# Kernel tuning notes

Measured on AMD Instinct MI355X. Metric: run time of the kernel, lower is better.

## Reference

```python
import jax, jax.numpy as jnp
import numpy as np

BATCH = 32768
DIM = 256
NUM_LATENTS = 4096
ENTROPY_WEIGHT = 0.1
VQ_BETA = 0.25
EPS = 1e-9


def _l2_normalize(v, axis=-1, eps=1e-12):
    # matches torch F.normalize(dim=-1)
    n = jnp.linalg.norm(v, axis=axis, keepdims=True)
    return v / jnp.maximum(n, eps)


def setup_inputs() -> dict:
    key = jax.random.key(0)
    kx, kc = jax.random.split(key)
    x = jax.random.normal(kx, (BATCH, DIM), dtype=jnp.float32)
    # codebook initialized uniform(-bound, bound) then row-normalized, as in __init__
    bound = (3.0 / DIM) ** 0.5
    cb = jax.random.uniform(kc, (NUM_LATENTS, DIM), dtype=jnp.float32,
                            minval=-bound, maxval=bound)
    codebook = _l2_normalize(cb)
    return {"x": x, "codebook": codebook}


def reference(x, codebook):
    # cosine-distance nearest-code lookup
    x_norm = _l2_normalize(x)                       # [B, D]
    cb_norm = _l2_normalize(codebook)               # [K, D]
    distance = -jnp.einsum('bd,kd->bk', x_norm, cb_norm)  # [B, K]
    # dropout p=0.0 -> identity
    indices = jnp.argmin(distance, axis=-1)         # [B] int
    z = codebook[indices]                           # [B, D] gather

    # straight-through estimator
    z_q = x + jax.lax.stop_gradient(z - x)

    commit_loss = jnp.mean((x - jax.lax.stop_gradient(z)) ** 2)
    q_loss = jnp.mean((z - jax.lax.stop_gradient(x)) ** 2)

    # entropy of codebook usage
    counts = jnp.bincount(indices, length=NUM_LATENTS).astype(jnp.float32)
    probs = counts / counts.sum()
    entropy = -jnp.sum(probs * jnp.log(jnp.clip(probs, EPS)))
    entropy_loss = -entropy

    vq_loss = q_loss + VQ_BETA * commit_loss + ENTROPY_WEIGHT * entropy_loss
    return (z_q, vq_loss, q_loss, commit_loss, entropy_loss, entropy, indices)
```

## Files before the change

kernel.cpp:

```cpp
#include <hip/hip_runtime.h>
#include <math.h>

#define BATCH 32768
#define DIM   256
#define NLAT  4096

typedef _Float16 f16x8 __attribute__((ext_vector_type(8)));
typedef float    f32x16 __attribute__((ext_vector_type(16)));

#define WS_CBH    0u
#define WS_CBINV  2097152u
#define WS_KEYS   2113536u
#define WS_HIST   4210688u

__device__ inline float kdec(uint key) {
  return __uint_as_float(key & 0xFFFFF000u);
}

__device__ inline void gload_lds16(const void* g, void* l) {
  __builtin_amdgcn_global_load_lds(
      (const __attribute__((address_space(1))) void*)g,
      (__attribute__((address_space(3))) void*)l, 16, 0, 0);
}

__global__ __launch_bounds__(256) void prep1_kernel(
    const float* __restrict__ cb, float* __restrict__ cbinv,
    int* __restrict__ hist) {
  int bid = blockIdx.x;
  if (bid < 1024) {
    int w = threadIdx.x >> 6, l = threadIdx.x & 63;
    int row = bid * 4 + w;
    const float4* cr = (const float4*)(cb + (size_t)row * DIM);
    float4 v = cr[l];
    float s = v.x * v.x + v.y * v.y + v.z * v.z + v.w * v.w;
    #pragma unroll
    for (int m = 32; m; m >>= 1) s += __shfl_xor(s, m, 64);
    if (l == 0) cbinv[row] = 1.0f / fmaxf(sqrtf(s), 1e-12f);
  } else {
    for (int k = threadIdx.x; k < NLAT; k += 256) hist[k] = 0;
  }
}

__global__ __launch_bounds__(256) void prep2_kernel(
    const float* __restrict__ x, const float* __restrict__ cb,
    const float* __restrict__ cbinv, uint4* __restrict__ cbhf4,
    uint4* __restrict__ xhf4) {
  int bid = blockIdx.x, tid = threadIdx.x;
  if (bid < 512) {
    int gid = bid * 256 + tid;
    int frag = gid >> 6, lane = gid & 63;
    int rf = frag & 1, ts = frag >> 1, sl = ts & 15, t = ts >> 4;
    int row = t * 64 + rf * 32 + (lane & 31);
    int e4 = sl * 4 + (lane >> 5) * 2;
    const float4* cr = (const float4*)(cb + (size_t)row * DIM);
    float inv = cbinv[row];
    float4 a = cr[e4], b = cr[e4 + 1];
    union { _Float16 h[8]; uint4 u; } pk;
    pk.h[0] = (_Float16)(a.x * inv); pk.h[1] = (_Float16)(a.y * inv);
    pk.h[2] = (_Float16)(a.z * inv); pk.h[3] = (_Float16)(a.w * inv);
    pk.h[4] = (_Float16)(b.x * inv); pk.h[5] = (_Float16)(b.y * inv);
    pk.h[6] = (_Float16)(b.z * inv); pk.h[7] = (_Float16)(b.w * inv);
    cbhf4[gid] = pk.u;
  } else {
    int o = (bid - 512) * 256 + tid;
    int rowgrp = o >> 10, rem = o & 1023;
    int sl = rem >> 6, rem2 = rem & 63;
    int lhh = rem2 >> 5, l31r = rem2 & 31;
    int row = rowgrp * 32 + l31r;
    int c = sl * 2 + lhh;
    const float4* xs = (const float4*)x;
    float4 a = xs[(size_t)row * 64 + c * 2];
    float4 b = xs[(size_t)row * 64 + c * 2 + 1];
    union { _Float16 h[8]; uint4 u; } pk;
    pk.h[0] = (_Float16)a.x; pk.h[1] = (_Float16)a.y;
    pk.h[2] = (_Float16)a.z; pk.h[3] = (_Float16)a.w;
    pk.h[4] = (_Float16)b.x; pk.h[5] = (_Float16)b.y;
    pk.h[6] = (_Float16)b.z; pk.h[7] = (_Float16)b.w;
    xhf4[o] = pk.u;
  }
}

__global__ __launch_bounds__(256, 2) void vq_gemm_kernel(
    const char* __restrict__ xhf, const char* __restrict__ cbhf,
    uint* __restrict__ keys) {
  __shared__ __align__(16) char smem[65536];

  const int tid = threadIdx.x;
  const int w = tid >> 6, l = tid & 63;
  const int l31 = l & 31, lh = l >> 5;
  const int bb = blockIdx.x >> 2, q = blockIdx.x & 3;
  const int wrow0 = bb * 256 + w * 64;
  const int cbase = q * 1024;
  const uint lh4u = (uint)(lh << 2);

  f16x8 xf[16][2];
  #pragma unroll
  for (int fc = 0; fc < 2; ++fc) {
    const char* xb = xhf + (size_t)(bb * 8 + w * 2 + fc) * 16384
                   + (size_t)l * 16;
    #pragma unroll
    for (int s2 = 0; s2 < 16; ++s2)
      xf[s2][fc] = *(const f16x8*)(xb + s2 * 1024);
  }

  const char* qbase = cbhf + (size_t)q * 524288;
  auto STAGE = [&](int bufoff, int t) {
    const char* src = qbase + t * 32768 + (size_t)tid * 16;
    char* dst = smem + bufoff + w * 1024;
    #pragma unroll
    for (int s = 0; s < 8; ++s)
      gload_lds16(src + s * 4096, dst + s * 4096);
  };

  STAGE(0, 0);
  asm volatile("s_waitcnt vmcnt(0)" ::: "memory");
  __syncthreads();

  uint k1[2] = {0, 0}, k2[2] = {0, 0}, k3[2] = {0, 0};
  int curoff = 0;

  #pragma unroll 1
  for (int t = 0; t < 16; ++t) {
    if (t < 15) STAGE(curoff ^ 32768, t + 1);

    f32x16 acc[2][2];
    #pragma unroll
    for (int rf = 0; rf < 2; ++rf)
      #pragma unroll
      for (int fc = 0; fc < 2; ++fc)
        #pragma unroll
        for (int r = 0; r < 16; ++r) acc[rf][fc][r] = 32.0f;

    const char* bp = smem + curoff + (size_t)l * 16;
    #pragma unroll
    for (int sl = 0; sl < 16; ++sl) {
      f16x8 a0 = *(const f16x8*)(bp + (sl * 2) * 1024);
      f16x8 a1 = *(const f16x8*)(bp + (sl * 2 + 1) * 1024);
      #pragma unroll
      for (int fc = 0; fc < 2; ++fc) {
        acc[0][fc] = __builtin_amdgcn_mfma_f32_32x32x16_f16(
            a0, xf[sl][fc], acc[0][fc], 0, 0, 0);
        acc[1][fc] = __builtin_amdgcn_mfma_f32_32x32x16_f16(
            a1, xf[sl][fc], acc[1][fc], 0, 0, 0);
      }
    }

    const uint scode = (uint)(cbase + t * 64);
    #pragma unroll
    for (int fc = 0; fc < 2; ++fc) {
      #pragma unroll
      for (int rf = 0; rf < 2; ++rf) {
        #pragma unroll
        for (int r = 0; r < 16; ++r) {
          const uint cr = (uint)(rf * 32 + (r & 3) + 8 * (r >> 2));
          uint key = (__float_as_uint(acc[rf][fc][r]) & 0xFFFFF000u)
                   | scode | cr | lh4u;
          uint m1 = max(k1[fc], key), n1 = min(k1[fc], key); k1[fc] = m1;
          uint m2 = max(k2[fc], n1),  n2 = min(k2[fc], n1);  k2[fc] = m2;
          k3[fc] = max(k3[fc], n2);
        }
      }
    }

    asm volatile("s_waitcnt vmcnt(0)" ::: "memory");
    __syncthreads();
    curoff ^= 32768;
  }

  #pragma unroll
  for (int fc = 0; fc < 2; ++fc) {
    uint a1 = k1[fc], a2 = k2[fc], a3 = k3[fc];
    uint o1 = __shfl_xor(a1, 32, 64);
    uint o2 = __shfl_xor(a2, 32, 64);
    uint o3 = __shfl_xor(a3, 32, 64);
    uint a4 = 0;
    #pragma unroll
    for (int e = 0; e < 3; ++e) {
      uint o = (e == 0) ? o1 : (e == 1) ? o2 : o3;
      uint m = max(a1, o), n = min(a1, o); a1 = m;
      m = max(a2, n); n = min(a2, n); a2 = m;
      m = max(a3, n); n = min(a3, n); a3 = m;
      a4 = max(a4, n);
    }
    if (lh == 0) {
      uint4 kv; kv.x = a1; kv.y = a2; kv.z = a3; kv.w = a4;
      *(uint4*)(keys + (size_t)(wrow0 + fc * 32 + l31) * 16 + q * 4) = kv;
    }
  }
}

__global__ __launch_bounds__(256) void rescore_kernel(
    const float* __restrict__ x, const float* __restrict__ cb,
    const float* __restrict__ cbinv, const uint* __restrict__ keys,
    float* __restrict__ zq, float* __restrict__ out_idx,
    int* __restrict__ hist, double* __restrict__ psse) {
  __shared__ float part[4];
  int tid = threadIdx.x, w = tid >> 6, l = tid & 63;
  int row = blockIdx.x * 4 + w;
  const float4* xr = (const float4*)(x + (size_t)row * DIM);
  float4 xv = xr[l];
  float s0 = xv.x * xv.x + xv.y * xv.y + xv.z * xv.z + xv.w * xv.w;
  #pragma unroll
  for (int m = 32; m; m >>= 1) s0 += __shfl_xor(s0, m, 64);
  float xnorm = sqrtf(s0);
  float xinv = 1.0f / fmaxf(xnorm, 1e-12f);

  uint key = keys[row * 16 + (l & 15)];
  uint kmax = key;
  #pragma unroll
  for (int m = 1; m < 16; m <<= 1) {
    uint o = __shfl_xor(kmax, m, 64);
    kmax = (o > kmax) ? o : kmax;
  }
  float dmax = kdec(kmax);
  float thr = dmax - 2.0f * (3e-3f * xnorm);
  bool inwin = (kdec(key) >= thr) && (l < 16);
  unsigned long long mask = __ballot(inwin);
  int besti;
  if (__popcll(mask) == 1) {
    besti = (int)(kmax & 0xFFFu);
  } else {
    float bestv = -3e38f; besti = 0x7fffffff;
    unsigned long long mm = mask;
    while (mm) {
      int b = __ffsll(mm) - 1; mm &= mm - 1;
      int ci = (int)(__shfl(key, b, 64) & 0xFFFu);
      float cbi = cbinv[ci];
      const float4* cr = (const float4*)(cb + (size_t)ci * DIM);
      float4 cv = cr[l];
      float d = (xv.x * xinv) * (cv.x * cbi) + (xv.y * xinv) * (cv.y * cbi)
              + (xv.z * xinv) * (cv.z * cbi) + (xv.w * xinv) * (cv.w * cbi);
      #pragma unroll
      for (int m = 32; m; m >>= 1) d += __shfl_xor(d, m, 64);
      bool better = (d > bestv) || (d == bestv && ci < besti);
      bestv = better ? d : bestv;
      besti = better ? ci : besti;
    }
  }

  float4 zv = ((const float4*)(cb + (size_t)besti * DIM))[l];
  float4 o;
  o.x = xv.x + (zv.x - xv.x); o.y = xv.y + (zv.y - xv.y);
  o.z = xv.z + (zv.z - xv.z); o.w = xv.w + (zv.w - xv.w);
  ((float4*)(zq + (size_t)row * DIM))[l] = o;
  float dx = xv.x - zv.x, dy = xv.y - zv.y, dz = xv.z - zv.z, dw = xv.w - zv.w;
  float s = dx * dx + dy * dy + dz * dz + dw * dw;
  #pragma unroll
  for (int m = 32; m; m >>= 1) s += __shfl_xor(s, m, 64);
  if (l == 0) part[w] = s;
  __syncthreads();
  if (tid == 0)
    psse[blockIdx.x] = (double)((part[0] + part[1]) + (part[2] + part[3]));
  if (l == 0) {
    atomicAdd(&hist[besti], 1);
    out_idx[row] = (float)besti;
  }
}

__global__ __launch_bounds__(256) void finalize_kernel(
    const int* __restrict__ hist, const double* __restrict__ psse,
    float* __restrict__ outs) {
  int tid = threadIdx.x;
  double e = 0.0, s = 0.0;
  for (int k = tid; k < NLAT; k += 256) {
    int c = hist[k];
    if (c > 0) {
      float p = (float)c * (1.0f / 32768.0f);
      e += (double)(p * logf(p));
    }
  }
  for (int k = tid; k < BATCH / 4; k += 256) s += psse[k];
  #pragma unroll
  for (int off = 32; off; off >>= 1) {
    e += __shfl_xor(e, off, 64);
    s += __shfl_xor(s, off, 64);
  }
  __shared__ double pe[4], ps[4];
  int w = tid >> 6, l = tid & 63;
  if (l == 0) { pe[w] = e; ps[w] = s; }
  __syncthreads();
  if (tid == 0) {
    double H = -((pe[0] + pe[1]) + (pe[2] + pe[3]));
    double sse = (ps[0] + ps[1]) + (ps[2] + ps[3]);
    double qv = sse * (1.0 / ((double)BATCH * (double)DIM));
    float qf = (float)qv;
    float Hf = (float)H;
    float ent_loss = -Hf;
    float vq = qf + 0.25f * qf + 0.1f * ent_loss;
    outs[0] = vq;
    outs[1] = qf;
    outs[2] = qf;
    outs[3] = ent_loss;
    outs[4] = Hf;
  }
}

extern "C" void kernel_launch(void* const* d_in, const int* in_sizes, int n_in,
                              void* d_out, int out_size, void* d_ws, size_t ws_size,
                              hipStream_t stream) {
  const float* x  = (const float*)d_in[0];
  const float* cb = (const float*)d_in[1];

  float* out     = (float*)d_out;
  float* zq      = out;
  float* scalars = out + (size_t)BATCH * DIM;
  float* oidx    = scalars + 5;

  char* wsb = (char*)d_ws;
  ushort* cbhf  = (ushort*)(wsb + WS_CBH);
  float*  cbinv = (float*)(wsb + WS_CBINV);
  uint*   keys  = (uint*)(wsb + WS_KEYS);
  int*    hist  = (int*)(wsb + WS_HIST);
  double* psse  = (double*)(wsb + WS_CBH);

  ushort* xhf = (ushort*)d_out;

  prep1_kernel<<<1025, 256, 0, stream>>>(cb, cbinv, hist);
  prep2_kernel<<<4608, 256, 0, stream>>>(x, cb, cbinv,
                                         (uint4*)cbhf, (uint4*)xhf);
  vq_gemm_kernel<<<512, 256, 0, stream>>>((const char*)xhf,
                                          (const char*)cbhf, keys);
  rescore_kernel<<<BATCH / 4, 256, 0, stream>>>(x, cb, cbinv, keys,
                                                zq, oidx, hist, psse);
  finalize_kernel<<<1, 256, 0, stream>>>(hist, psse, scalars);
}
```

Baseline: 200.8 us.

## Deepen GEMM codebook pipeline to four half-tile buffers and coalesce x conversion

The GEMM kernel now stages the codebook in 16KB half-tiles across a four-slot LDS ring with three stages in flight, using partial vmcnt waits instead of full drains. MFMA sections run at raised wave priority. The x fp16 conversion now reads rows contiguously and transposes the fragment layout through LDS, using fewer blocks, so global reads are coalesced. This adds more barriers per tile and relies on the vmcnt counting being correct for the ring.

```diff
diff --git a/kernel.cpp b/kernel.cpp
--- a/kernel.cpp
+++ b/kernel.cpp
@@ -46,8 +46,29 @@
     const float* __restrict__ cbinv, uint4* __restrict__ cbhf4,
     uint4* __restrict__ xhf4) {
   int bid = blockIdx.x, tid = threadIdx.x;
-  if (bid < 512) {
-    int gid = bid * 256 + tid;
+  if (bid < 1024) {
+    __shared__ __align__(16) uint4 lds[1024];
+    const float4* xs = (const float4*)x + (size_t)bid * 2048;
+    #pragma unroll
+    for (int k = 0; k < 4; ++k) {
+      int g = tid * 4 + k;
+      float4 a = xs[g * 2];
+      float4 b = xs[g * 2 + 1];
+      union { _Float16 h[8]; uint4 u; } pk;
+      pk.h[0] = (_Float16)a.x; pk.h[1] = (_Float16)a.y;
+      pk.h[2] = (_Float16)a.z; pk.h[3] = (_Float16)a.w;
+      pk.h[4] = (_Float16)b.x; pk.h[5] = (_Float16)b.y;
+      pk.h[6] = (_Float16)b.z; pk.h[7] = (_Float16)b.w;
+      int row31 = g >> 5, c = g & 31;
+      lds[(c >> 1) * 64 + (c & 1) * 32 + row31] = pk.u;
+    }
+    __syncthreads();
+    uint4* outp = xhf4 + (size_t)bid * 1024;
+    #pragma unroll
+    for (int k = 0; k < 4; ++k)
+      outp[tid * 4 + k] = lds[tid * 4 + k];
+  } else {
+    int gid = (bid - 1024) * 256 + tid;
     int frag = gid >> 6, lane = gid & 63;
     int rf = frag & 1, ts = frag >> 1, sl = ts & 15, t = ts >> 4;
     int row = t * 64 + rf * 32 + (lane & 31);
@@ -61,22 +82,6 @@
     pk.h[4] = (_Float16)(b.x * inv); pk.h[5] = (_Float16)(b.y * inv);
     pk.h[6] = (_Float16)(b.z * inv); pk.h[7] = (_Float16)(b.w * inv);
     cbhf4[gid] = pk.u;
-  } else {
-    int o = (bid - 512) * 256 + tid;
-    int rowgrp = o >> 10, rem = o & 1023;
-    int sl = rem >> 6, rem2 = rem & 63;
-    int lhh = rem2 >> 5, l31r = rem2 & 31;
-    int row = rowgrp * 32 + l31r;
-    int c = sl * 2 + lhh;
-    const float4* xs = (const float4*)x;
-    float4 a = xs[(size_t)row * 64 + c * 2];
-    float4 b = xs[(size_t)row * 64 + c * 2 + 1];
-    union { _Float16 h[8]; uint4 u; } pk;
-    pk.h[0] = (_Float16)a.x; pk.h[1] = (_Float16)a.y;
-    pk.h[2] = (_Float16)a.z; pk.h[3] = (_Float16)a.w;
-    pk.h[4] = (_Float16)b.x; pk.h[5] = (_Float16)b.y;
-    pk.h[6] = (_Float16)b.z; pk.h[7] = (_Float16)b.w;
-    xhf4[o] = pk.u;
   }
 }
 
@@ -104,45 +109,70 @@
   }
 
   const char* qbase = cbhf + (size_t)q * 524288;
-  auto STAGE = [&](int bufoff, int t) {
-    const char* src = qbase + t * 32768 + (size_t)tid * 16;
-    char* dst = smem + bufoff + w * 1024;
-    #pragma unroll
-    for (int s = 0; s < 8; ++s)
+  auto STAGE = [&](int h) {
+    const char* src = qbase + h * 16384 + (size_t)tid * 16;
+    char* dst = smem + (h & 3) * 16384 + w * 1024;
+    #pragma unroll
+    for (int s = 0; s < 4; ++s)
       gload_lds16(src + s * 4096, dst + s * 4096);
   };
 
-  STAGE(0, 0);
   asm volatile("s_waitcnt vmcnt(0)" ::: "memory");
-  __syncthreads();
+  STAGE(0); STAGE(1); STAGE(2);
 
   uint k1[2] = {0, 0}, k2[2] = {0, 0}, k3[2] = {0, 0};
-  int curoff = 0;
 
   #pragma unroll 1
   for (int t = 0; t < 16; ++t) {
-    if (t < 15) STAGE(curoff ^ 32768, t + 1);
-
     f32x16 acc[2][2];
+
+    STAGE((2 * t + 3) & 31);
+    asm volatile("s_waitcnt vmcnt(12)" ::: "memory");
+    __syncthreads();
     #pragma unroll
     for (int rf = 0; rf < 2; ++rf)
       #pragma unroll
       for (int fc = 0; fc < 2; ++fc)
         #pragma unroll
         for (int r = 0; r < 16; ++r) acc[rf][fc][r] = 32.0f;
-
-    const char* bp = smem + curoff + (size_t)l * 16;
-    #pragma unroll
-    for (int sl = 0; sl < 16; ++sl) {
-      f16x8 a0 = *(const f16x8*)(bp + (sl * 2) * 1024);
-      f16x8 a1 = *(const f16x8*)(bp + (sl * 2 + 1) * 1024);
-      #pragma unroll
-      for (int fc = 0; fc < 2; ++fc) {
-        acc[0][fc] = __builtin_amdgcn_mfma_f32_32x32x16_f16(
-            a0, xf[sl][fc], acc[0][fc], 0, 0, 0);
-        acc[1][fc] = __builtin_amdgcn_mfma_f32_32x32x16_f16(
-            a1, xf[sl][fc], acc[1][fc], 0, 0, 0);
+    {
+      const char* bp = smem + ((2 * t) & 3) * 16384 + (size_t)l * 16;
+      __builtin_amdgcn_s_setprio(1);
+      #pragma unroll
+      for (int s8 = 0; s8 < 8; ++s8) {
+        f16x8 a0 = *(const f16x8*)(bp + s8 * 2048);
+        f16x8 a1 = *(const f16x8*)(bp + s8 * 2048 + 1024);
+        #pragma unroll
+        for (int fc = 0; fc < 2; ++fc) {
+          acc[0][fc] = __builtin_amdgcn_mfma_f32_32x32x16_f16(
+              a0, xf[s8][fc], acc[0][fc], 0, 0, 0);
+          acc[1][fc] = __builtin_amdgcn_mfma_f32_32x32x16_f16(
+              a1, xf[s8][fc], acc[1][fc], 0, 0, 0);
+        }
       }
+      __builtin_amdgcn_s_setprio(0);
+    }
+    __syncthreads();
+
+    STAGE((2 * t + 4) & 31);
+    asm volatile("s_waitcnt vmcnt(12)" ::: "memory");
+    __syncthreads();
+    {
+      const char* bp = smem + ((2 * t + 1) & 3) * 16384 + (size_t)l * 16;
+      __builtin_amdgcn_s_setprio(1);
+      #pragma unroll
+      for (int s8 = 0; s8 < 8; ++s8) {
+        f16x8 a0 = *(const f16x8*)(bp + s8 * 2048);
+        f16x8 a1 = *(const f16x8*)(bp + s8 * 2048 + 1024);
+        #pragma unroll
+        for (int fc = 0; fc < 2; ++fc) {
+          acc[0][fc] = __builtin_amdgcn_mfma_f32_32x32x16_f16(
+              a0, xf[8 + s8][fc], acc[0][fc], 0, 0, 0);
+          acc[1][fc] = __builtin_amdgcn_mfma_f32_32x32x16_f16(
+              a1, xf[8 + s8][fc], acc[1][fc], 0, 0, 0);
+        }
+      }
+      __builtin_amdgcn_s_setprio(0);
     }
 
     const uint scode = (uint)(cbase + t * 64);
@@ -161,11 +191,9 @@
         }
       }
     }
-
-    asm volatile("s_waitcnt vmcnt(0)" ::: "memory");
-    __syncthreads();
-    curoff ^= 32768;
-  }
+    __syncthreads();
+  }
+  asm volatile("s_waitcnt vmcnt(0)" ::: "memory");
 
   #pragma unroll
   for (int fc = 0; fc < 2; ++fc) {
@@ -316,7 +344,7 @@
   ushort* xhf = (ushort*)d_out;
 
   prep1_kernel<<<1025, 256, 0, stream>>>(cb, cbinv, hist);
-  prep2_kernel<<<4608, 256, 0, stream>>>(x, cb, cbinv,
+  prep2_kernel<<<1536, 256, 0, stream>>>(x, cb, cbinv,
                                          (uint4*)cbhf, (uint4*)xhf);
   vq_gemm_kernel<<<512, 256, 0, stream>>>((const char*)xhf,
                                           (const char*)cbhf, keys);
```

Result: no change. 200.6 us (-0.1%).
